# Optimization experiments

Hardware: AMD Instinct MI355X
Metric: run time of the kernel (lower is better)

Reference implementation:

```python
import jax, jax.numpy as jnp
import numpy as np

N_SPH = 7
N_RAD = 6
CUTOFF = 5.0
P = 5  # envelope exponent
E = 500000
T = 2000000

# ---- numpy-side precompute of spherical Bessel roots & normalizers ----
# matches sympy bessel_basis(n,k): basis[l][j] = N_{l,j} * j_l(z_{l,j} * x)

def _sph_jn_np(t, l):
    t = np.asarray(t, dtype=np.float64)
    j0 = np.sin(t) / t
    if l == 0:
        return j0
    j1 = np.sin(t) / t**2 - np.cos(t) / t
    for i in range(2, l + 1):
        j0, j1 = j1, (2 * i - 1) / t * j1 - j0
    return j1


def _jn_zeros(n, k):
    # k-th zeros of spherical bessel j_l for l=0..n-1, via interlacing + bisection
    nz = k + n - 1
    zeros = np.zeros((n, nz))
    zeros[0] = np.arange(1, nz + 1) * np.pi  # zeros of j_0
    for l in range(1, n):
        for i in range(nz - l):
            a, b = zeros[l - 1, i], zeros[l - 1, i + 1]
            fa = _sph_jn_np(a, l)
            for _ in range(80):
                m = 0.5 * (a + b)
                fm = _sph_jn_np(m, l)
                if fa * fm <= 0:
                    b = m
                else:
                    a, fa = m, fm
            zeros[l, i] = 0.5 * (a + b)
    return zeros[:, :k]

_Z = _jn_zeros(N_SPH, N_RAD)  # [n, k]
_NORM = np.sqrt(2.0) / np.abs(np.stack([_sph_jn_np(_Z[l], l + 1) for l in range(N_SPH)]))
FREQ = jnp.asarray(_Z, dtype=jnp.float32)   # [n, k]
NORM = jnp.asarray(_NORM, dtype=jnp.float32)  # [n, k]
# real sph harm (m=0): Y_l(theta) = sqrt((2l+1)/4pi) * P_l(cos theta)
Y_COEF = jnp.asarray(np.sqrt((2 * np.arange(N_SPH) + 1) / (4 * np.pi)), dtype=jnp.float32)


def _sph_jn(t, l):
    j0 = jnp.sin(t) / t
    if l == 0:
        return j0
    j1 = jnp.sin(t) / t**2 - jnp.cos(t) / t
    for i in range(2, l + 1):
        j0, j1 = j1, (2 * i - 1) / t * j1 - j0
    return j1


def _forward(dist, angle, idx_kj):
    n, k = N_SPH, N_RAD
    x = dist / CUTOFF  # [E]
    # radial basis: [E, n*k], layout l-major / j-minor like torch stack order
    rbf = jnp.concatenate(
        [NORM[l] * _sph_jn(x[:, None] * FREQ[l], l) for l in range(n)], axis=1)
    # envelope (DimeNet variant: no cutoff masking)
    a = -(P + 1) * (P + 2) / 2.0
    b = float(P * (P + 2))
    c = -P * (P + 1) / 2.0
    xp = x**P
    env = 1.0 / x + a * xp + b * xp * x + c * xp * x * x
    rbf = env[:, None] * rbf
    # angular basis via Legendre recurrence on cos(theta)
    cth = jnp.cos(angle)
    Ps = [jnp.ones_like(cth), cth]
    for l in range(2, n):
        Ps.append(((2 * l - 1) * cth * Ps[-1] - (l - 1) * Ps[-2]) / l)
    cbf = jnp.stack([Y_COEF[l] * Ps[l] for l in range(n)], axis=1)  # [T, n]
    out = (rbf[idx_kj].reshape(-1, n, k) * cbf[:, :, None]).reshape(-1, n * k)
    return out


def setup_inputs() -> dict:
    key = jax.random.key(0)
    k1, k2, k3 = jax.random.split(key, 3)
    # distances kept away from 0 (envelope has 1/x term)
    dist = jax.random.uniform(k1, (E,), jnp.float32, 0.1, 1.0) * CUTOFF
    angle = jax.random.uniform(k2, (T,), jnp.float32, 0.0, float(np.pi))
    idx_kj = jax.random.randint(k3, (T,), 0, E)
    return {"dist": dist, "angle": angle, "idx_kj": idx_kj}


def reference(dist, angle, idx_kj):
    return _forward(dist, angle, idx_kj)
```

## Files before the change

### kernel.cpp

```cpp
#include <hip/hip_runtime.h>
#include <hip/hip_bf16.h>
#include <cmath>

#define N_SPH 7
#define N_RAD 6
#define NC (N_SPH * N_RAD)
#define INV_CUTOFF 0.2f

typedef float f2 __attribute__((ext_vector_type(2)));
typedef float f4 __attribute__((ext_vector_type(4)));

struct BesselConsts {
    float freq[NC];
    float norm[NC];
    float ycoef[N_SPH];
};

static double h_sph_jn(double t, int l) {
    double j0 = sin(t) / t;
    if (l == 0) return j0;
    double j1 = sin(t) / (t * t) - cos(t) / t;
    for (int i = 2; i <= l; i++) {
        double j2 = (2.0 * i - 1.0) / t * j1 - j0;
        j0 = j1; j1 = j2;
    }
    return j1;
}

static void compute_consts(BesselConsts* bc) {
    const int n = N_SPH, k = N_RAD, nz = N_RAD + N_SPH - 1;
    const double PI = 3.14159265358979323846;
    double zeros[N_SPH][12];
    for (int i = 0; i < nz; i++) zeros[0][i] = (i + 1) * PI;
    for (int l = 1; l < n; l++) {
        for (int i = 0; i < nz - l; i++) {
            double a = zeros[l - 1][i], b = zeros[l - 1][i + 1];
            double fa = h_sph_jn(a, l);
            for (int it = 0; it < 80; it++) {
                double m = 0.5 * (a + b);
                double fm = h_sph_jn(m, l);
                if (fa * fm <= 0.0) { b = m; } else { a = m; fa = fm; }
            }
            zeros[l][i] = 0.5 * (a + b);
        }
    }
    for (int l = 0; l < n; l++)
        for (int j = 0; j < k; j++) {
            bc->freq[l * k + j] = (float)zeros[l][j];
            bc->norm[l * k + j] =
                (float)(sqrt(2.0) / fabs(h_sph_jn(zeros[l][j], l + 1)));
        }
    for (int l = 0; l < n; l++)
        bc->ycoef[l] = (float)sqrt((2.0 * l + 1.0) / (4.0 * PI));
}

__global__ __launch_bounds__(256) void rbf_kernel(
    const float* __restrict__ dist, float* __restrict__ rbf, int E_,
    BesselConsts bc) {
    __shared__ __align__(16) float stage[256 * NC];
    const int tix = threadIdx.x;
    const int e0 = blockIdx.x * 256;
    const int e = e0 + tix;
    const bool valid = e < E_;
    float x = valid ? dist[e] * INV_CUTOFF : 0.5f;
    float xp = x * x * x * x * x;
    float env = 1.0f / x + xp * (-21.0f + x * (35.0f - 15.0f * x));

#pragma unroll
    for (int l = 0; l < N_SPH; ++l) {
#pragma unroll
        for (int j = 0; j < N_RAD; ++j) {
            const int c = l * N_RAD + j;
            float tt = x * bc.freq[c];
            float s, co;
            sincosf(tt, &s, &co);
            float rf = 1.0f / tt;
            double r = (double)rf;
            r = r * (2.0 - (double)tt * r);
            double jv;
            double j0 = (double)s * r;
            if (l == 0) {
                jv = j0;
            } else {
                double j1 = ((double)s * r - (double)co) * r;
#pragma unroll
                for (int i = 2; i <= l; ++i) {
                    double j2 = (2.0 * i - 1.0) * r * j1 - j0;
                    j0 = j1; j1 = j2;
                }
                jv = j1;
            }
            stage[tix * NC + c] = env * bc.norm[c] * (float)jv;
        }
    }
    __syncthreads();
    const int rows = min(256, E_ - e0);
    const int nelem = rows * NC;
    const int n4 = nelem >> 2;
    const size_t base = (size_t)e0 * NC;
#pragma unroll
    for (int it = 0; it < 11; ++it) {
        int i = it * 256 + tix;
        if (i < n4) {
            f4 v = *reinterpret_cast<const f4*>(&stage[4 * i]);
            *reinterpret_cast<f4*>(rbf + base + 4 * (size_t)i) = v;
        }
    }
    for (int i = n4 * 4 + tix; i < nelem; i += 256) rbf[base + i] = stage[i];
}

__global__ __launch_bounds__(256) void out_kernel(
    const float* __restrict__ angle, const int* __restrict__ idx,
    const float* __restrict__ rbf, float* __restrict__ out, int T_,
    BesselConsts bc) {
    __shared__ float yP[256 * 8];
    __shared__ int sidx[256];
    const int tix = threadIdx.x;
    const int t0 = blockIdx.x * 256;
    const int t = t0 + tix;

    float cth = 0.0f;
    int id = 0;
    if (t < T_) {
        cth = cosf(angle[t]);
        id = idx[t];
    }
    float P[N_SPH];
    P[0] = 1.0f;
    P[1] = cth;
#pragma unroll
    for (int l = 2; l < N_SPH; ++l)
        P[l] = ((2 * l - 1) * cth * P[l - 1] - (l - 1) * P[l - 2]) *
               (1.0f / (float)l);
#pragma unroll
    for (int l = 0; l < N_SPH; ++l) yP[tix * 8 + l] = bc.ycoef[l] * P[l];
    sidx[tix] = id;
    __syncthreads();

    const int rows = min(256, T_ - t0);
    const int npair = rows * (NC / 2);
    const size_t base = (size_t)t0 * NC;
#pragma unroll
    for (int it = 0; it < NC / 2; ++it) {
        int pi = it * 256 + tix;
        if (pi < npair) {
            unsigned row = (unsigned)pi / 21u;
            unsigned c = 2u * ((unsigned)pi - row * 21u);
            unsigned l = c / 6u;
            const f2 rv =
                *reinterpret_cast<const f2*>(rbf + (size_t)sidx[row] * NC + c);
            float y = yP[row * 8 + l];
            f2 o;
            o.x = y * rv.x;
            o.y = y * rv.y;
            __builtin_nontemporal_store(
                o, reinterpret_cast<f2*>(out + base + 2 * (size_t)pi));
        }
    }
}

__global__ __launch_bounds__(256) void fused_kernel(
    const float* __restrict__ dist, const float* __restrict__ angle,
    const int* __restrict__ idx, float* __restrict__ out, int ntot,
    BesselConsts bc) {
    int tid = blockIdx.x * 256 + threadIdx.x;
    if (tid >= ntot) return;
    int t = tid / NC;
    int c = tid - t * NC;
    int l = c / N_RAD;
    int e = idx[t];
    float x = dist[e] * INV_CUTOFF;
    float tt = x * bc.freq[c];
    float s, co;
    sincosf(tt, &s, &co);
    double r = 1.0 / (double)tt;
    double j0 = (double)s * r, jv;
    if (l == 0) jv = j0;
    else {
        double j1 = ((double)s * r - (double)co) * r;
        for (int i = 2; i <= l; ++i) {
            double j2 = (2.0 * i - 1.0) * r * j1 - j0;
            j0 = j1; j1 = j2;
        }
        jv = j1;
    }
    float xp = x * x * x * x * x;
    float env = 1.0f / x + xp * (-21.0f + x * (35.0f - 15.0f * x));
    float p0 = 1.0f, p1 = cosf(angle[t]), pl = (l == 0) ? 1.0f : p1;
    for (int i = 2; i <= l; ++i) {
        float p2 = ((2 * i - 1) * p1 * cosf(angle[t]) - (i - 1) * p0) / i;
        p0 = p1; p1 = p2; pl = p2;
    }
    out[tid] = bc.ycoef[l] * pl * env * bc.norm[c] * (float)jv;
}

extern "C" void kernel_launch(void* const* d_in, const int* in_sizes, int n_in,
                              void* d_out, int out_size, void* d_ws,
                              size_t ws_size, hipStream_t stream) {
    const float* dist = (const float*)d_in[0];
    const float* angle = (const float*)d_in[1];
    const int* idx = (const int*)d_in[2];
    float* out = (float*)d_out;

    int E_ = in_sizes[0];
    int T_ = in_sizes[1];
    int na = E_ * NC;
    int nb = T_ * NC;

    BesselConsts bc;
    compute_consts(&bc);

    if (ws_size >= (size_t)na * sizeof(float)) {
        float* rbf = (float*)d_ws;
        rbf_kernel<<<(E_ + 255) / 256, 256, 0, stream>>>(dist, rbf, E_, bc);
        out_kernel<<<(T_ + 255) / 256, 256, 0, stream>>>(angle, idx, rbf, out,
                                                         T_, bc);
    } else {
        fused_kernel<<<(nb + 255) / 256, 256, 0, stream>>>(dist, angle, idx,
                                                           out, nb, bc);
    }
}
```

Measured before the change: 445.9 us.

## Fuse radial basis and gather into a single per-triplet kernel

Replaces the two-kernel scheme with a single kernel that recomputes the radial Bessel basis for every triplet. The old scheme materialised an intermediate rbf table in workspace and then gathered random rows from it; the new kernel reads dist[idx[t]] directly and folds in the angular factor. This removes the intermediate buffer's write and the random gather reads, and stages output rows in LDS for coalesced nontemporal stores. In exchange, sincos and the double-precision recurrence now run for every triplet rather than once per edge, roughly four times as much transcendental and FP64 work.

After: 418.2 us. -6.2%, faster.

```diff
diff --git a/kernel.cpp b/kernel.cpp
--- a/kernel.cpp
+++ b/kernel.cpp
@@ -54,17 +54,33 @@
         bc->ycoef[l] = (float)sqrt((2.0 * l + 1.0) / (4.0 * PI));
 }
 
-__global__ __launch_bounds__(256) void rbf_kernel(
-    const float* __restrict__ dist, float* __restrict__ rbf, int E_,
+__global__ __launch_bounds__(256) void fused_row_kernel(
+    const float* __restrict__ dist, const float* __restrict__ angle,
+    const int* __restrict__ idx, float* __restrict__ out, int T_,
     BesselConsts bc) {
     __shared__ __align__(16) float stage[256 * NC];
     const int tix = threadIdx.x;
-    const int e0 = blockIdx.x * 256;
-    const int e = e0 + tix;
-    const bool valid = e < E_;
-    float x = valid ? dist[e] * INV_CUTOFF : 0.5f;
+    const int t0 = blockIdx.x * 256;
+    const int t = t0 + tix;
+    const bool valid = t < T_;
+
+    float x = 0.5f, cth = 0.0f;
+    if (valid) {
+        x = dist[idx[t]] * INV_CUTOFF;
+        cth = cosf(angle[t]);
+    }
     float xp = x * x * x * x * x;
     float env = 1.0f / x + xp * (-21.0f + x * (35.0f - 15.0f * x));
+    float P[N_SPH];
+    P[0] = 1.0f;
+    P[1] = cth;
+#pragma unroll
+    for (int l = 2; l < N_SPH; ++l)
+        P[l] = ((2 * l - 1) * cth * P[l - 1] - (l - 1) * P[l - 2]) *
+               (1.0f / (float)l);
+    float yP[N_SPH];
+#pragma unroll
+    for (int l = 0; l < N_SPH; ++l) yP[l] = bc.ycoef[l] * P[l];
 
 #pragma unroll
     for (int l = 0; l < N_SPH; ++l) {
@@ -90,108 +106,26 @@
                 }
                 jv = j1;
             }
-            stage[tix * NC + c] = env * bc.norm[c] * (float)jv;
+            stage[tix * NC + c] = yP[l] * (env * bc.norm[c] * (float)jv);
         }
     }
     __syncthreads();
-    const int rows = min(256, E_ - e0);
+
+    const int rows = min(256, T_ - t0);
     const int nelem = rows * NC;
     const int n4 = nelem >> 2;
-    const size_t base = (size_t)e0 * NC;
+    const size_t base = (size_t)t0 * NC;
 #pragma unroll
     for (int it = 0; it < 11; ++it) {
         int i = it * 256 + tix;
         if (i < n4) {
             f4 v = *reinterpret_cast<const f4*>(&stage[4 * i]);
-            *reinterpret_cast<f4*>(rbf + base + 4 * (size_t)i) = v;
+            __builtin_nontemporal_store(
+                v, reinterpret_cast<f4*>(out + base + 4 * (size_t)i));
         }
     }
-    for (int i = n4 * 4 + tix; i < nelem; i += 256) rbf[base + i] = stage[i];
-}
-
-__global__ __launch_bounds__(256) void out_kernel(
-    const float* __restrict__ angle, const int* __restrict__ idx,
-    const float* __restrict__ rbf, float* __restrict__ out, int T_,
-    BesselConsts bc) {
-    __shared__ float yP[256 * 8];
-    __shared__ int sidx[256];
-    const int tix = threadIdx.x;
-    const int t0 = blockIdx.x * 256;
-    const int t = t0 + tix;
-
-    float cth = 0.0f;
-    int id = 0;
-    if (t < T_) {
-        cth = cosf(angle[t]);
-        id = idx[t];
-    }
-    float P[N_SPH];
-    P[0] = 1.0f;
-    P[1] = cth;
-#pragma unroll
-    for (int l = 2; l < N_SPH; ++l)
-        P[l] = ((2 * l - 1) * cth * P[l - 1] - (l - 1) * P[l - 2]) *
-               (1.0f / (float)l);
-#pragma unroll
-    for (int l = 0; l < N_SPH; ++l) yP[tix * 8 + l] = bc.ycoef[l] * P[l];
-    sidx[tix] = id;
-    __syncthreads();
-
-    const int rows = min(256, T_ - t0);
-    const int npair = rows * (NC / 2);
-    const size_t base = (size_t)t0 * NC;
-#pragma unroll
-    for (int it = 0; it < NC / 2; ++it) {
-        int pi = it * 256 + tix;
-        if (pi < npair) {
-            unsigned row = (unsigned)pi / 21u;
-            unsigned c = 2u * ((unsigned)pi - row * 21u);
-            unsigned l = c / 6u;
-            const f2 rv =
-                *reinterpret_cast<const f2*>(rbf + (size_t)sidx[row] * NC + c);
-            float y = yP[row * 8 + l];
-            f2 o;
-            o.x = y * rv.x;
-            o.y = y * rv.y;
-            __builtin_nontemporal_store(
-                o, reinterpret_cast<f2*>(out + base + 2 * (size_t)pi));
-        }
-    }
-}
-
-__global__ __launch_bounds__(256) void fused_kernel(
-    const float* __restrict__ dist, const float* __restrict__ angle,
-    const int* __restrict__ idx, float* __restrict__ out, int ntot,
-    BesselConsts bc) {
-    int tid = blockIdx.x * 256 + threadIdx.x;
-    if (tid >= ntot) return;
-    int t = tid / NC;
-    int c = tid - t * NC;
-    int l = c / N_RAD;
-    int e = idx[t];
-    float x = dist[e] * INV_CUTOFF;
-    float tt = x * bc.freq[c];
-    float s, co;
-    sincosf(tt, &s, &co);
-    double r = 1.0 / (double)tt;
-    double j0 = (double)s * r, jv;
-    if (l == 0) jv = j0;
-    else {
-        double j1 = ((double)s * r - (double)co) * r;
-        for (int i = 2; i <= l; ++i) {
-            double j2 = (2.0 * i - 1.0) * r * j1 - j0;
-            j0 = j1; j1 = j2;
-        }
-        jv = j1;
-    }
-    float xp = x * x * x * x * x;
-    float env = 1.0f / x + xp * (-21.0f + x * (35.0f - 15.0f * x));
-    float p0 = 1.0f, p1 = cosf(angle[t]), pl = (l == 0) ? 1.0f : p1;
-    for (int i = 2; i <= l; ++i) {
-        float p2 = ((2 * i - 1) * p1 * cosf(angle[t]) - (i - 1) * p0) / i;
-        p0 = p1; p1 = p2; pl = p2;
-    }
-    out[tid] = bc.ycoef[l] * pl * env * bc.norm[c] * (float)jv;
+    for (int i = n4 * 4 + tix; i < nelem; i += 256)
+        __builtin_nontemporal_store(stage[i], out + base + i);
 }
 
 extern "C" void kernel_launch(void* const* d_in, const int* in_sizes, int n_in,
@@ -204,19 +138,11 @@
 
     int E_ = in_sizes[0];
     int T_ = in_sizes[1];
-    int na = E_ * NC;
-    int nb = T_ * NC;
+    (void)E_; (void)d_ws; (void)ws_size;
 
     BesselConsts bc;
     compute_consts(&bc);
 
-    if (ws_size >= (size_t)na * sizeof(float)) {
-        float* rbf = (float*)d_ws;
-        rbf_kernel<<<(E_ + 255) / 256, 256, 0, stream>>>(dist, rbf, E_, bc);
-        out_kernel<<<(T_ + 255) / 256, 256, 0, stream>>>(angle, idx, rbf, out,
-                                                         T_, bc);
-    } else {
-        fused_kernel<<<(nb + 255) / 256, 256, 0, stream>>>(dist, angle, idx,
-                                                           out, nb, bc);
-    }
+    fused_row_kernel<<<(T_ + 255) / 256, 256, 0, stream>>>(dist, angle, idx,
+                                                           out, T_, bc);
 }
```
